# Optimization experiments

Measured on AMD Instinct MI355X. Metric: run time of the kernel, lower is better.

Reference implementation:

```python
import jax, jax.numpy as jnp
import numpy as np

N_NODES = 100000
N_EDGES = 1600000
IN_DIM = 128
OUT_DIM = 64


def setup_inputs() -> dict:
    key = jax.random.key(0)
    k1, k2, k3, k4, k5, k6 = jax.random.split(key, 6)
    x = jax.random.normal(k1, (N_NODES, IN_DIM), dtype=jnp.float32)
    edge_row = jax.random.randint(k2, (N_EDGES,), 0, N_NODES, dtype=jnp.int32)
    edge_col = jax.random.randint(k3, (N_EDGES,), 0, N_NODES, dtype=jnp.int32)
    edge_val = jax.random.uniform(k4, (N_EDGES,), dtype=jnp.float32)
    W = jax.random.normal(k5, (IN_DIM, OUT_DIM), dtype=jnp.float32) * (1.0 / np.sqrt(IN_DIM))
    b = jax.random.normal(k6, (OUT_DIM,), dtype=jnp.float32) * 0.01
    return {"x": x, "edge_row": edge_row, "edge_col": edge_col,
            "edge_val": edge_val, "W": W, "b": b}


def reference(x, edge_row, edge_col, edge_val, W, b):
    # xw = Linear(x)  -> [N, OUT_DIM]
    xw = x @ W + b
    # SpMM: (A_hat @ xw)[r] = sum_e val[e] * xw[col[e]] for edges with row[e]==r
    msgs = edge_val[:, None] * xw[edge_col]          # [E, OUT_DIM]
    ax = jax.ops.segment_sum(msgs, edge_row, num_segments=N_NODES)  # [N, OUT_DIM]
    # ReLU; dropout p=0.0 is identity (eval mode)
    return jax.nn.relu(ax)
```

## Files before the change

### kernel.cpp

```cpp
#include <hip/hip_runtime.h>
#include <hip/hip_fp16.h>
#include <limits.h>

#define IN_DIM 128
#define OUT_DIM 64
#define NBUCK 782
#define RPB 128
#define HRPB 64
#define CHUNK 4096
#define BCAP 4096
#define SCAP2 2048


typedef _Float16 half8_t __attribute__((ext_vector_type(8)));
typedef float    f32x4  __attribute__((ext_vector_type(4)));

__device__ __forceinline__ int kmap(int g, int j) {
    return g * 4 + (j & 3) + 16 * (j >> 2);
}

__global__ __launch_bounds__(256) void gemm_kernel(
    const float* __restrict__ x, const float* __restrict__ W,
    const float* __restrict__ b, __half* __restrict__ xw, int n_nodes) {
    const int t  = threadIdx.x;
    const int l  = t & 63;
    const int wv = t >> 6;
    const int g  = l >> 4;
    const int rowbase = blockIdx.x * 64 + wv * 16;
    const int row = rowbase + (l & 15);
    const bool rok = row < n_nodes;
    const float* xr = x + (size_t)row * IN_DIM;

    half8_t bf[4][4];
    #pragma unroll
    for (int n = 0; n < 4; ++n)
        #pragma unroll
        for (int ks = 0; ks < 4; ++ks) {
            half8_t a;
            #pragma unroll
            for (int j = 0; j < 8; ++j) {
                const int k = ks * 32 + kmap(g, j);
                a[j] = (_Float16)W[k * OUT_DIM + n * 16 + (l & 15)];
            }
            bf[n][ks] = a;
        }

    half8_t af[4];
    #pragma unroll
    for (int ks = 0; ks < 4; ++ks) {
        float4 c0 = rok ? *(const float4*)(xr + ks * 32 + g * 4)
                        : make_float4(0.f, 0.f, 0.f, 0.f);
        float4 c1 = rok ? *(const float4*)(xr + ks * 32 + 16 + g * 4)
                        : make_float4(0.f, 0.f, 0.f, 0.f);
        half8_t a;
        a[0] = (_Float16)c0.x; a[1] = (_Float16)c0.y;
        a[2] = (_Float16)c0.z; a[3] = (_Float16)c0.w;
        a[4] = (_Float16)c1.x; a[5] = (_Float16)c1.y;
        a[6] = (_Float16)c1.z; a[7] = (_Float16)c1.w;
        af[ks] = a;
    }

    f32x4 acc[4];
    #pragma unroll
    for (int n = 0; n < 4; ++n) acc[n] = (f32x4){0.f, 0.f, 0.f, 0.f};

    #pragma unroll
    for (int ks = 0; ks < 4; ++ks)
        #pragma unroll
        for (int n = 0; n < 4; ++n)
            acc[n] = __builtin_amdgcn_mfma_f32_16x16x32_f16(af[ks], bf[n][ks], acc[n], 0, 0, 0);

    float bias[4];
    #pragma unroll
    for (int n = 0; n < 4; ++n) bias[n] = b[n * 16 + (l & 15)];

    #pragma unroll
    for (int n = 0; n < 4; ++n)
        #pragma unroll
        for (int q = 0; q < 4; ++q) {
            const int ro = rowbase + g * 4 + q;
            if (ro < n_nodes)
                xw[(size_t)ro * OUT_DIM + n * 16 + (l & 15)] =
                    __float2half(acc[n][q] + bias[n]);
        }
}

__global__ __launch_bounds__(512) void partition_kernel(
    const int* __restrict__ erow, const int* __restrict__ ecol,
    const float* __restrict__ eval_, int* __restrict__ cursor,
    int2* __restrict__ ecs, int n_edges) {
    __shared__ int  hist[NBUCK];
    __shared__ int  lbase[NBUCK];
    __shared__ int  gdelta[NBUCK];
    __shared__ int2 data[CHUNK];
    __shared__ int  gpos[CHUNK];
    __shared__ int  wsum[8];

    const int t = threadIdx.x;
    const int base = blockIdx.x * CHUNK;
    const int cnt = min(CHUNK, n_edges - base);

    for (int i = t; i < NBUCK; i += 512) hist[i] = 0;
    __syncthreads();

    int   myrow[CHUNK / 512];
    int   mycol[CHUNK / 512];
    float myval[CHUNK / 512];
    #pragma unroll
    for (int i = 0; i < CHUNK / 512; ++i) {
        const int idx = t + i * 512;
        if (idx < cnt) {
            const int e = base + idx;
            myrow[i] = erow[e];
            mycol[i] = ecol[e];
            myval[i] = eval_[e];
            atomicAdd(&hist[myrow[i] >> 7], 1);
        }
    }
    __syncthreads();

    {
        const int i0 = 2 * t, i1 = 2 * t + 1;
        const int v0 = (i0 < NBUCK) ? hist[i0] : 0;
        const int v1 = (i1 < NBUCK) ? hist[i1] : 0;
        const int s2 = v0 + v1;
        int inc = s2;
        #pragma unroll
        for (int d = 1; d < 64; d <<= 1) {
            int u = __shfl_up(inc, d, 64);
            if ((t & 63) >= d) inc += u;
        }
        if ((t & 63) == 63) wsum[t >> 6] = inc;
        __syncthreads();
        int wp = 0;
        #pragma unroll
        for (int w = 0; w < 8; ++w) if (w < (t >> 6)) wp += wsum[w];
        const int ex = wp + (inc - s2);
        if (i0 < NBUCK) lbase[i0] = ex;
        if (i1 < NBUCK) lbase[i1] = ex + v0;
    }
    __syncthreads();

    for (int i = t; i < NBUCK; i += 512) {
        const int c = hist[i];
        gdelta[i] = c ? (i * BCAP + atomicAdd(&cursor[i], c) - lbase[i]) : 0;
    }
    __syncthreads();

    #pragma unroll
    for (int i = 0; i < CHUNK / 512; ++i) {
        const int idx = t + i * 512;
        if (idx < cnt) {
            const int bk = myrow[i] >> 7;
            const int slot = atomicAdd(&lbase[bk], 1);
            int2 p;
            p.x = (int)(((unsigned)(myrow[i] & (RPB - 1)) << 25) |
                        ((unsigned)mycol[i] << 7));
            p.y = __float_as_int(myval[i]);
            data[slot] = p;
            gpos[slot] = slot + gdelta[bk];
        }
    }
    __syncthreads();

    const int limit = NBUCK * BCAP - 1;
    for (int slot = t; slot < cnt; slot += 512)
        ecs[min(gpos[slot], limit)] = data[slot];
}

__global__ __launch_bounds__(512) void bucket_gather_kernel(
    const __half* __restrict__ xw, const int2* __restrict__ ecs,
    const int* __restrict__ cursor, float* __restrict__ out,
    int n_nodes) {
    __shared__ int2 data[SCAP2];
    __shared__ int  hist[HRPB];
    __shared__ int  rstart[HRPB + 1];

    const int bk2  = blockIdx.x;
    const int bk   = bk2 >> 1;
    const int half = bk2 & 1;
    const int t    = threadIdx.x;
    const int lane = t & 63;
    const int wv   = t >> 6;
    const int q    = lane & 7;
    const int g    = lane >> 3;

    const int s   = bk * BCAP;
    const int cnt = min(cursor[bk], BCAP);
    const int e   = s + cnt;
    const int rowbase = bk * RPB + half * HRPB;
    const char* xwb = (const char*)xw;

    if (t < HRPB) hist[t] = 0;
    __syncthreads();

    for (int i = t; i < cnt; i += 512) {
        const unsigned rl = ((unsigned)ecs[s + i].x) >> 25;
        if ((int)(rl >> 6) == half) atomicAdd(&hist[rl & (HRPB - 1)], 1);
    }
    __syncthreads();

    if (t < HRPB) {
        const int v = hist[t];
        int inc = v;
        #pragma unroll
        for (int d = 1; d < 64; d <<= 1) {
            int u = __shfl_up(inc, d, 64);
            if (t >= d) inc += u;
        }
        rstart[t] = inc - v;
        hist[t]   = inc - v;
        if (t == HRPB - 1) rstart[HRPB] = inc;
    }
    __syncthreads();

    const int cntH = rstart[HRPB];

    if (cntH <= SCAP2) {
        for (int i = t; i < cnt; i += 512) {
            const int2 p = ecs[s + i];
            const unsigned rl = ((unsigned)p.x) >> 25;
            if ((int)(rl >> 6) == half) {
                const int pos = atomicAdd(&hist[rl & (HRPB - 1)], 1);
                data[pos] = p;
            }
        }
        __syncthreads();

        for (int rp = 0; rp < 4; ++rp) {
            const int rl0 = wv * 8 + rp * 2;
            const int rl1 = rl0 + 1;
            int j0 = rstart[rl0];
            const int e0 = rstart[rl0 + 1];
            int j1 = rstart[rl1];
            const int e1 = rstart[rl1 + 1];

            float acc0[8], acc1[8];
            #pragma unroll
            for (int i = 0; i < 8; ++i) { acc0[i] = 0.f; acc1[i] = 0.f; }

            while (j0 < e0 || j1 < e1) {
                const bool a0 = j0 < e0;
                const bool a1 = j1 < e1;
                float v0 = 0.f, v1 = 0.f;
                unsigned off0 = 0, off1 = 0;
                if (a0) {
                    const int ei = j0 + g;
                    const int2 p = data[min(ei, cntH - 1)];
                    v0 = (ei < e0) ? __int_as_float(p.y) : 0.f;
                    off0 = (((unsigned)p.x) & 0x01FFFF80u) | ((unsigned)q << 4);
                }
                if (a1) {
                    const int ei = j1 + g;
                    const int2 p = data[min(ei, cntH - 1)];
                    v1 = (ei < e1) ? __int_as_float(p.y) : 0.f;
                    off1 = (((unsigned)p.x) & 0x01FFFF80u) | ((unsigned)q << 4);
                }
                union { uint4 u; __half2 h[4]; } U0, U1;
                if (a0) U0.u = *(const uint4*)(xwb + off0);
                if (a1) U1.u = *(const uint4*)(xwb + off1);
                if (a0) {
                    #pragma unroll
                    for (int i = 0; i < 4; ++i) {
                        const float2 f = __half22float2(U0.h[i]);
                        acc0[2 * i]     = fmaf(v0, f.x, acc0[2 * i]);
                        acc0[2 * i + 1] = fmaf(v0, f.y, acc0[2 * i + 1]);
                    }
                    j0 += 8;
                }
                if (a1) {
                    #pragma unroll
                    for (int i = 0; i < 4; ++i) {
                        const float2 f = __half22float2(U1.h[i]);
                        acc1[2 * i]     = fmaf(v1, f.x, acc1[2 * i]);
                        acc1[2 * i + 1] = fmaf(v1, f.y, acc1[2 * i + 1]);
                    }
                    j1 += 8;
                }
            }

            #pragma unroll
            for (int d = 8; d < 64; d <<= 1) {
                #pragma unroll
                for (int i = 0; i < 8; ++i) {
                    acc0[i] += __shfl_xor(acc0[i], d, 64);
                    acc1[i] += __shfl_xor(acc1[i], d, 64);
                }
            }

            if (g == 0) {
                const int r0 = rowbase + rl0;
                const int r1 = rowbase + rl1;
                if (r0 < n_nodes) {
                    float4 o0, o1;
                    o0.x = fmaxf(acc0[0], 0.f); o0.y = fmaxf(acc0[1], 0.f);
                    o0.z = fmaxf(acc0[2], 0.f); o0.w = fmaxf(acc0[3], 0.f);
                    o1.x = fmaxf(acc0[4], 0.f); o1.y = fmaxf(acc0[5], 0.f);
                    o1.z = fmaxf(acc0[6], 0.f); o1.w = fmaxf(acc0[7], 0.f);
                    float* op = out + (size_t)r0 * OUT_DIM + q * 8;
                    *(float4*)(op)     = o0;
                    *(float4*)(op + 4) = o1;
                }
                if (r1 < n_nodes) {
                    float4 o0, o1;
                    o0.x = fmaxf(acc1[0], 0.f); o0.y = fmaxf(acc1[1], 0.f);
                    o0.z = fmaxf(acc1[2], 0.f); o0.w = fmaxf(acc1[3], 0.f);
                    o1.x = fmaxf(acc1[4], 0.f); o1.y = fmaxf(acc1[5], 0.f);
                    o1.z = fmaxf(acc1[6], 0.f); o1.w = fmaxf(acc1[7], 0.f);
                    float* op = out + (size_t)r1 * OUT_DIM + q * 8;
                    *(float4*)(op)     = o0;
                    *(float4*)(op + 4) = o1;
                }
            }
        }
    } else {
        for (int rr = 0; rr < 8; ++rr) {
            const int r = rowbase + wv * 8 + rr;
            if (r >= n_nodes) break;
            float acc[8];
            #pragma unroll
            for (int i = 0; i < 8; ++i) acc[i] = 0.f;
            const unsigned rl = (unsigned)(r & (RPB - 1));
            for (int j = s + g; j < e; j += 8) {
                const int2 p = ecs[j];
                if ((((unsigned)p.x) >> 25) == rl) {
                    const float v = __int_as_float(p.y);
                    const unsigned off = (((unsigned)p.x) & 0x01FFFF80u) | ((unsigned)q << 4);
                    union { uint4 u; __half2 h[4]; } U;
                    U.u = *(const uint4*)(xwb + off);
                    #pragma unroll
                    for (int i = 0; i < 4; ++i) {
                        const float2 f = __half22float2(U.h[i]);
                        acc[2 * i]     = fmaf(v, f.x, acc[2 * i]);
                        acc[2 * i + 1] = fmaf(v, f.y, acc[2 * i + 1]);
                    }
                }
            }
            #pragma unroll
            for (int d = 8; d < 64; d <<= 1)
                #pragma unroll
                for (int i = 0; i < 8; ++i)
                    acc[i] += __shfl_xor(acc[i], d, 64);
            if (g == 0) {
                float4 o0, o1;
                o0.x = fmaxf(acc[0], 0.f); o0.y = fmaxf(acc[1], 0.f);
                o0.z = fmaxf(acc[2], 0.f); o0.w = fmaxf(acc[3], 0.f);
                o1.x = fmaxf(acc[4], 0.f); o1.y = fmaxf(acc[5], 0.f);
                o1.z = fmaxf(acc[6], 0.f); o1.w = fmaxf(acc[7], 0.f);
                float* op = out + (size_t)r * OUT_DIM + q * 8;
                *(float4*)(op)     = o0;
                *(float4*)(op + 4) = o1;
            }
        }
    }
}

__global__ __launch_bounds__(256) void edge_scatter_kernel(
    const __half* __restrict__ xw, const int* __restrict__ erow,
    const int* __restrict__ ecol, const float* __restrict__ eval_,
    float* __restrict__ out, int n_edges) {
    const int lane  = threadIdx.x & 63;
    const int wid   = (blockIdx.x * blockDim.x + threadIdx.x) >> 6;
    const int nwave = (gridDim.x * blockDim.x) >> 6;
    for (int e = wid; e < n_edges; e += nwave) {
        const float m = eval_[e] * __half2float(xw[(size_t)ecol[e] * OUT_DIM + lane]);
        atomicAdd(&out[(size_t)erow[e] * OUT_DIM + lane], m);
    }
}

__global__ __launch_bounds__(256) void relu_kernel(float4* __restrict__ p, int n4) {
    const int stride = gridDim.x * blockDim.x;
    for (int i = blockIdx.x * blockDim.x + threadIdx.x; i < n4; i += stride) {
        float4 v = p[i];
        v.x = fmaxf(v.x, 0.f); v.y = fmaxf(v.y, 0.f);
        v.z = fmaxf(v.z, 0.f); v.w = fmaxf(v.w, 0.f);
        p[i] = v;
    }
}

extern "C" void kernel_launch(void* const* d_in, const int* in_sizes, int n_in,
                              void* d_out, int out_size, void* d_ws, size_t ws_size,
                              hipStream_t stream) {
    const float* x     = (const float*)d_in[0];
    const int*   erow  = (const int*)d_in[1];
    const int*   ecol  = (const int*)d_in[2];
    const float* eval_ = (const float*)d_in[3];
    const float* W     = (const float*)d_in[4];
    const float* b     = (const float*)d_in[5];
    float*       out   = (float*)d_out;

    const int n_nodes = in_sizes[0] / IN_DIM;
    const int n_edges = in_sizes[1];

    auto align256 = [](size_t v) { return (v + 255) & ~(size_t)255; };
    size_t off_xw     = 0;
    size_t off_cursor = align256(off_xw     + (size_t)n_nodes * OUT_DIM * 2);
    size_t off_ecs    = align256(off_cursor + (size_t)NBUCK * 4);
    size_t need       = off_ecs + (size_t)NBUCK * BCAP * 8;

    __half* xw = (__half*)((char*)d_ws + off_xw);

    const bool main_path = (need <= ws_size) && (n_nodes <= NBUCK * RPB) && (n_edges > 0);

    if (main_path) {
        int*  cursor = (int*)((char*)d_ws + off_cursor);
        int2* ecs    = (int2*)((char*)d_ws + off_ecs);

        hipMemsetAsync(cursor, 0, (size_t)NBUCK * 4, stream);
        gemm_kernel<<<(n_nodes + 63) / 64, 256, 0, stream>>>(x, W, b, xw, n_nodes);
        partition_kernel<<<(n_edges + CHUNK - 1) / CHUNK, 512, 0, stream>>>(
            erow, ecol, eval_, cursor, ecs, n_edges);
        bucket_gather_kernel<<<NBUCK * 2, 512, 0, stream>>>(
            xw, ecs, cursor, out, n_nodes);
    } else {
        gemm_kernel<<<(n_nodes + 63) / 64, 256, 0, stream>>>(x, W, b, xw, n_nodes);
        hipMemsetAsync(d_out, 0, (size_t)out_size * sizeof(float), stream);
        edge_scatter_kernel<<<8192, 256, 0, stream>>>(xw, erow, ecol, eval_, out, n_edges);
        relu_kernel<<<2048, 256, 0, stream>>>((float4*)d_out, out_size / 4);
    }
}
```

Measured before the change: 101.4 us.

## Fuse GEMM and edge partition into one launch with interleaved block roles

Merges the independent linear-layer GEMM and the edge bucketing partition into a single kernel, with blocks interleaved between the two roles so both run concurrently on the GPU. The aim is to drop one launch and the serialization gap between the two independent stages, overlapping the compute-bound GEMM with the atomic-heavy partition. CHUNK is halved to 2048, giving more partition blocks and less shared memory per block, at the cost of more global cursor atomics. GEMM blocks now cover 128 rows with 512 threads but carry the partition's shared-memory footprint, which may reduce occupancy.

```diff
diff --git a/kernel.cpp b/kernel.cpp
--- a/kernel.cpp
+++ b/kernel.cpp
@@ -7,7 +7,7 @@
 #define NBUCK 782
 #define RPB 128
 #define HRPB 64
-#define CHUNK 4096
+#define CHUNK 2048
 #define BCAP 4096
 #define SCAP2 2048
 
@@ -19,76 +19,12 @@
     return g * 4 + (j & 3) + 16 * (j >> 2);
 }
 
-__global__ __launch_bounds__(256) void gemm_kernel(
+__global__ __launch_bounds__(512) void fused_gemm_part_kernel(
     const float* __restrict__ x, const float* __restrict__ W,
-    const float* __restrict__ b, __half* __restrict__ xw, int n_nodes) {
-    const int t  = threadIdx.x;
-    const int l  = t & 63;
-    const int wv = t >> 6;
-    const int g  = l >> 4;
-    const int rowbase = blockIdx.x * 64 + wv * 16;
-    const int row = rowbase + (l & 15);
-    const bool rok = row < n_nodes;
-    const float* xr = x + (size_t)row * IN_DIM;
-
-    half8_t bf[4][4];
-    #pragma unroll
-    for (int n = 0; n < 4; ++n)
-        #pragma unroll
-        for (int ks = 0; ks < 4; ++ks) {
-            half8_t a;
-            #pragma unroll
-            for (int j = 0; j < 8; ++j) {
-                const int k = ks * 32 + kmap(g, j);
-                a[j] = (_Float16)W[k * OUT_DIM + n * 16 + (l & 15)];
-            }
-            bf[n][ks] = a;
-        }
-
-    half8_t af[4];
-    #pragma unroll
-    for (int ks = 0; ks < 4; ++ks) {
-        float4 c0 = rok ? *(const float4*)(xr + ks * 32 + g * 4)
-                        : make_float4(0.f, 0.f, 0.f, 0.f);
-        float4 c1 = rok ? *(const float4*)(xr + ks * 32 + 16 + g * 4)
-                        : make_float4(0.f, 0.f, 0.f, 0.f);
-        half8_t a;
-        a[0] = (_Float16)c0.x; a[1] = (_Float16)c0.y;
-        a[2] = (_Float16)c0.z; a[3] = (_Float16)c0.w;
-        a[4] = (_Float16)c1.x; a[5] = (_Float16)c1.y;
-        a[6] = (_Float16)c1.z; a[7] = (_Float16)c1.w;
-        af[ks] = a;
-    }
-
-    f32x4 acc[4];
-    #pragma unroll
-    for (int n = 0; n < 4; ++n) acc[n] = (f32x4){0.f, 0.f, 0.f, 0.f};
-
-    #pragma unroll
-    for (int ks = 0; ks < 4; ++ks)
-        #pragma unroll
-        for (int n = 0; n < 4; ++n)
-            acc[n] = __builtin_amdgcn_mfma_f32_16x16x32_f16(af[ks], bf[n][ks], acc[n], 0, 0, 0);
-
-    float bias[4];
-    #pragma unroll
-    for (int n = 0; n < 4; ++n) bias[n] = b[n * 16 + (l & 15)];
-
-    #pragma unroll
-    for (int n = 0; n < 4; ++n)
-        #pragma unroll
-        for (int q = 0; q < 4; ++q) {
-            const int ro = rowbase + g * 4 + q;
-            if (ro < n_nodes)
-                xw[(size_t)ro * OUT_DIM + n * 16 + (l & 15)] =
-                    __float2half(acc[n][q] + bias[n]);
-        }
-}
-
-__global__ __launch_bounds__(512) void partition_kernel(
+    const float* __restrict__ b, __half* __restrict__ xw, int n_nodes, int ngb,
     const int* __restrict__ erow, const int* __restrict__ ecol,
     const float* __restrict__ eval_, int* __restrict__ cursor,
-    int2* __restrict__ ecs, int n_edges) {
+    int2* __restrict__ ecs, int n_edges, int npb) {
     __shared__ int  hist[NBUCK];
     __shared__ int  lbase[NBUCK];
     __shared__ int  gdelta[NBUCK];
@@ -96,76 +32,147 @@
     __shared__ int  gpos[CHUNK];
     __shared__ int  wsum[8];
 
+    const int bid = blockIdx.x;
+    const int nm  = min(ngb, npb);
+    int role, idx;
+    if (bid < 2 * nm) { role = bid & 1; idx = bid >> 1; }
+    else              { idx = bid - nm; role = (ngb > nm) ? 0 : 1; }
+
     const int t = threadIdx.x;
-    const int base = blockIdx.x * CHUNK;
-    const int cnt = min(CHUNK, n_edges - base);
-
-    for (int i = t; i < NBUCK; i += 512) hist[i] = 0;
-    __syncthreads();
-
-    int   myrow[CHUNK / 512];
-    int   mycol[CHUNK / 512];
-    float myval[CHUNK / 512];
-    #pragma unroll
-    for (int i = 0; i < CHUNK / 512; ++i) {
-        const int idx = t + i * 512;
-        if (idx < cnt) {
-            const int e = base + idx;
-            myrow[i] = erow[e];
-            mycol[i] = ecol[e];
-            myval[i] = eval_[e];
-            atomicAdd(&hist[myrow[i] >> 7], 1);
-        }
-    }
-    __syncthreads();
-
-    {
-        const int i0 = 2 * t, i1 = 2 * t + 1;
-        const int v0 = (i0 < NBUCK) ? hist[i0] : 0;
-        const int v1 = (i1 < NBUCK) ? hist[i1] : 0;
-        const int s2 = v0 + v1;
-        int inc = s2;
-        #pragma unroll
-        for (int d = 1; d < 64; d <<= 1) {
-            int u = __shfl_up(inc, d, 64);
-            if ((t & 63) >= d) inc += u;
-        }
-        if ((t & 63) == 63) wsum[t >> 6] = inc;
-        __syncthreads();
-        int wp = 0;
-        #pragma unroll
-        for (int w = 0; w < 8; ++w) if (w < (t >> 6)) wp += wsum[w];
-        const int ex = wp + (inc - s2);
-        if (i0 < NBUCK) lbase[i0] = ex;
-        if (i1 < NBUCK) lbase[i1] = ex + v0;
-    }
-    __syncthreads();
-
-    for (int i = t; i < NBUCK; i += 512) {
-        const int c = hist[i];
-        gdelta[i] = c ? (i * BCAP + atomicAdd(&cursor[i], c) - lbase[i]) : 0;
-    }
-    __syncthreads();
-
-    #pragma unroll
-    for (int i = 0; i < CHUNK / 512; ++i) {
-        const int idx = t + i * 512;
-        if (idx < cnt) {
-            const int bk = myrow[i] >> 7;
-            const int slot = atomicAdd(&lbase[bk], 1);
-            int2 p;
-            p.x = (int)(((unsigned)(myrow[i] & (RPB - 1)) << 25) |
-                        ((unsigned)mycol[i] << 7));
-            p.y = __float_as_int(myval[i]);
-            data[slot] = p;
-            gpos[slot] = slot + gdelta[bk];
-        }
-    }
-    __syncthreads();
-
-    const int limit = NBUCK * BCAP - 1;
-    for (int slot = t; slot < cnt; slot += 512)
-        ecs[min(gpos[slot], limit)] = data[slot];
+
+    if (role == 0) {
+        const int l  = t & 63;
+        const int wv = t >> 6;
+        const int g  = l >> 4;
+        const int rowbase = idx * 128 + wv * 16;
+        const int row = rowbase + (l & 15);
+        const bool rok = row < n_nodes;
+        const float* xr = x + (size_t)row * IN_DIM;
+
+        half8_t bf[4][4];
+        #pragma unroll
+        for (int n = 0; n < 4; ++n)
+            #pragma unroll
+            for (int ks = 0; ks < 4; ++ks) {
+                half8_t a;
+                #pragma unroll
+                for (int j = 0; j < 8; ++j) {
+                    const int k = ks * 32 + kmap(g, j);
+                    a[j] = (_Float16)W[k * OUT_DIM + n * 16 + (l & 15)];
+                }
+                bf[n][ks] = a;
+            }
+
+        half8_t af[4];
+        #pragma unroll
+        for (int ks = 0; ks < 4; ++ks) {
+            float4 c0 = rok ? *(const float4*)(xr + ks * 32 + g * 4)
+                            : make_float4(0.f, 0.f, 0.f, 0.f);
+            float4 c1 = rok ? *(const float4*)(xr + ks * 32 + 16 + g * 4)
+                            : make_float4(0.f, 0.f, 0.f, 0.f);
+            half8_t a;
+            a[0] = (_Float16)c0.x; a[1] = (_Float16)c0.y;
+            a[2] = (_Float16)c0.z; a[3] = (_Float16)c0.w;
+            a[4] = (_Float16)c1.x; a[5] = (_Float16)c1.y;
+            a[6] = (_Float16)c1.z; a[7] = (_Float16)c1.w;
+            af[ks] = a;
+        }
+
+        f32x4 acc[4];
+        #pragma unroll
+        for (int n = 0; n < 4; ++n) acc[n] = (f32x4){0.f, 0.f, 0.f, 0.f};
+
+        #pragma unroll
+        for (int ks = 0; ks < 4; ++ks)
+            #pragma unroll
+            for (int n = 0; n < 4; ++n)
+                acc[n] = __builtin_amdgcn_mfma_f32_16x16x32_f16(af[ks], bf[n][ks], acc[n], 0, 0, 0);
+
+        float bias[4];
+        #pragma unroll
+        for (int n = 0; n < 4; ++n) bias[n] = b[n * 16 + (l & 15)];
+
+        #pragma unroll
+        for (int n = 0; n < 4; ++n)
+            #pragma unroll
+            for (int q = 0; q < 4; ++q) {
+                const int ro = rowbase + g * 4 + q;
+                if (ro < n_nodes)
+                    xw[(size_t)ro * OUT_DIM + n * 16 + (l & 15)] =
+                        __float2half(acc[n][q] + bias[n]);
+            }
+    } else {
+        const int base = idx * CHUNK;
+        const int cnt = min(CHUNK, n_edges - base);
+        if (cnt <= 0) return;
+
+        for (int i = t; i < NBUCK; i += 512) hist[i] = 0;
+        __syncthreads();
+
+        int   myrow[CHUNK / 512];
+        int   mycol[CHUNK / 512];
+        float myval[CHUNK / 512];
+        #pragma unroll
+        for (int i = 0; i < CHUNK / 512; ++i) {
+            const int j = t + i * 512;
+            if (j < cnt) {
+                const int e = base + j;
+                myrow[i] = erow[e];
+                mycol[i] = ecol[e];
+                myval[i] = eval_[e];
+                atomicAdd(&hist[myrow[i] >> 7], 1);
+            }
+        }
+        __syncthreads();
+
+        {
+            const int i0 = 2 * t, i1 = 2 * t + 1;
+            const int v0 = (i0 < NBUCK) ? hist[i0] : 0;
+            const int v1 = (i1 < NBUCK) ? hist[i1] : 0;
+            const int s2 = v0 + v1;
+            int inc = s2;
+            #pragma unroll
+            for (int d = 1; d < 64; d <<= 1) {
+                int u = __shfl_up(inc, d, 64);
+                if ((t & 63) >= d) inc += u;
+            }
+            if ((t & 63) == 63) wsum[t >> 6] = inc;
+            __syncthreads();
+            int wp = 0;
+            #pragma unroll
+            for (int w = 0; w < 8; ++w) if (w < (t >> 6)) wp += wsum[w];
+            const int ex = wp + (inc - s2);
+            if (i0 < NBUCK) lbase[i0] = ex;
+            if (i1 < NBUCK) lbase[i1] = ex + v0;
+        }
+        __syncthreads();
+
+        for (int i = t; i < NBUCK; i += 512) {
+            const int c = hist[i];
+            gdelta[i] = c ? (i * BCAP + atomicAdd(&cursor[i], c) - lbase[i]) : 0;
+        }
+        __syncthreads();
+
+        #pragma unroll
+        for (int i = 0; i < CHUNK / 512; ++i) {
+            const int j = t + i * 512;
+            if (j < cnt) {
+                const int bk = myrow[i] >> 7;
+                const int slot = atomicAdd(&lbase[bk], 1);
+                int2 p;
+                p.x = (int)(((unsigned)(myrow[i] & (RPB - 1)) << 25) |
+                            ((unsigned)mycol[i] << 7));
+                p.y = __float_as_int(myval[i]);
+                data[slot] = p;
+                gpos[slot] = slot + gdelta[bk];
+            }
+        }
+        __syncthreads();
+
+        const int limit = NBUCK * BCAP - 1;
+        for (int slot = t; slot < cnt; slot += 512)
+            ecs[min(gpos[slot], limit)] = data[slot];
+    }
 }
 
 __global__ __launch_bounds__(512) void bucket_gather_kernel(
@@ -400,20 +407,25 @@
 
     __half* xw = (__half*)((char*)d_ws + off_xw);
 
+    const int ngb = (n_nodes + 127) / 128;
+
     const bool main_path = (need <= ws_size) && (n_nodes <= NBUCK * RPB) && (n_edges > 0);
 
     if (main_path) {
         int*  cursor = (int*)((char*)d_ws + off_cursor);
         int2* ecs    = (int2*)((char*)d_ws + off_ecs);
+        const int npb = (n_edges + CHUNK - 1) / CHUNK;
 
         hipMemsetAsync(cursor, 0, (size_t)NBUCK * 4, stream);
-        gemm_kernel<<<(n_nodes + 63) / 64, 256, 0, stream>>>(x, W, b, xw, n_nodes);
-        partition_kernel<<<(n_edges + CHUNK - 1) / CHUNK, 512, 0, stream>>>(
-            erow, ecol, eval_, cursor, ecs, n_edges);
+        fused_gemm_part_kernel<<<ngb + npb, 512, 0, stream>>>(
+            x, W, b, xw, n_nodes, ngb,
+            erow, ecol, eval_, cursor, ecs, n_edges, npb);
         bucket_gather_kernel<<<NBUCK * 2, 512, 0, stream>>>(
             xw, ecs, cursor, out, n_nodes);
     } else {
-        gemm_kernel<<<(n_nodes + 63) / 64, 256, 0, stream>>>(x, W, b, xw, n_nodes);
+        fused_gemm_part_kernel<<<ngb, 512, 0, stream>>>(
+            x, W, b, xw, n_nodes, ngb,
+            nullptr, nullptr, nullptr, nullptr, nullptr, 0, 0);
         hipMemsetAsync(d_out, 0, (size_t)out_size * sizeof(float), stream);
         edge_scatter_kernel<<<8192, 256, 0, stream>>>(xw, erow, ecol, eval_, out, n_edges);
         relu_kernel<<<2048, 256, 0, stream>>>((float4*)d_out, out_size / 4);
```

Measured after the change: 102.2 us. Within noise of the previous version (+0.8%).
